# Optimization experiments

Hardware: AMD Instinct MI355X
Metric: run time of the kernel (lower is better)

## Reference

```python
import jax, jax.numpy as jnp
import numpy as np

HID = 512; NH = 8; HD = 64          # attention dims
SH = 8; SD = 32; SDIM = 256          # delta-state dims
NL = 6; FFN = 1536; VOC = 63
THETA = 500000.0; EPS = 1e-6


def rmsnorm(x, w, eps=EPS):
    xf = x.astype(jnp.float32)
    n = xf * jax.lax.rsqrt(jnp.mean(xf * xf, axis=-1, keepdims=True) + eps)
    return (n * w).astype(x.dtype)


def rotate_half(x):
    x1, x2 = jnp.split(x, 2, axis=-1)
    return jnp.concatenate([-x2, x1], axis=-1)


def delta_state(h, S0, Wk, Wv, Wq, Wbw, Wbb, Waw, Wab, Wout, nw, gw):
    # Gated delta-rule associative memory. h: (B,L,HID), S0: (B,SH,SD,SD)
    B, L, _ = h.shape
    k = (h @ Wk.T).reshape(B, L, SH, SD)
    v = (h @ Wv.T).reshape(B, L, SH, SD)
    q = (h @ Wq.T).reshape(B, L, SH, SD)
    beta = jax.nn.sigmoid(h @ Wbw.T + Wbb).reshape(B, L, SH, SD)
    alpha = jax.nn.sigmoid(h @ Waw.T + Wab).reshape(B, L, SH, SD)
    k = k / jnp.maximum(jnp.linalg.norm(k, axis=-1, keepdims=True), 1e-12)
    gate = h @ gw.T  # (B,L,SDIM)
    xs = tuple(jnp.moveaxis(a, 1, 0) for a in (k, v, q, beta, alpha))  # (L,B,SH,SD)

    def step(S, inp):
        k_t, v_t, q_t, b_t, a_t = inp
        S = S * a_t[..., None]                                  # decay rows
        pred = jnp.einsum('bhij,bhj->bhi', S, k_t)
        S = S + jnp.einsum('bhi,bhj->bhij', b_t * (v_t - pred), k_t)
        return S, jnp.einsum('bhij,bhj->bhi', S, q_t)

    S, reads = jax.lax.scan(step, S0, xs)
    ctx = jnp.moveaxis(reads, 0, 1).reshape(B, L, SDIM)
    ctx = rmsnorm(ctx, nw) * jax.nn.silu(gate)
    return ctx @ Wout.T, S


def attention(h, cos, sin, wq, wk, wv, wo):
    B, L, _ = h.shape
    q = (h @ wq.T).reshape(B, L, NH, HD).transpose(0, 2, 1, 3)
    k = (h @ wk.T).reshape(B, L, NH, HD).transpose(0, 2, 1, 3)
    v = (h @ wv.T).reshape(B, L, NH, HD).transpose(0, 2, 1, 3)
    c, s = cos[None, None], sin[None, None]
    q = q * c + rotate_half(q) * s
    k = k * c + rotate_half(k) * s
    scores = jnp.einsum('bhqd,bhkd->bhqk', q, k) / np.float32(np.sqrt(HD))
    mask = jnp.tril(jnp.ones((L, L), bool))
    scores = jnp.where(mask, scores, jnp.float32(-1e9))
    a = jax.nn.softmax(scores, axis=-1)
    o = jnp.einsum('bhqk,bhkd->bhqd', a, v).transpose(0, 2, 1, 3).reshape(B, L, HID)
    return o @ wo.T


def rope_tables(L, dtype):
    inv_freq = 1.0 / THETA ** (np.arange(0, HD, 2, dtype=np.float32) / HD)
    t = np.arange(L, dtype=np.float32)
    freqs = np.outer(t, inv_freq)
    emb = np.concatenate([freqs, freqs], axis=-1)
    return jnp.asarray(np.cos(emb), dtype), jnp.asarray(np.sin(emb), dtype)


def setup_inputs() -> dict:
    key = jax.random.key(0)
    ks = jax.random.split(key, 40)
    p = lambda i, shp: jax.random.normal(ks[i], shp, jnp.float32) * 0.02
    inp = {
        'input_ids': jax.random.randint(ks[0], (4, 1024), 0, VOC),
        'state': jnp.zeros((4, SH, SD, SD), jnp.float32),
        'embed': p(1, (VOC, HID)),
    }
    for j, pre in enumerate(['sr_', 'sw_']):
        b = 2 + j * 10
        inp[pre + 'Wk'] = p(b, (SDIM, HID)); inp[pre + 'Wv'] = p(b + 1, (SDIM, HID))
        inp[pre + 'Wq'] = p(b + 2, (SDIM, HID)); inp[pre + 'Wbw'] = p(b + 3, (SDIM, HID))
        inp[pre + 'Wbb'] = jnp.zeros((SDIM,), jnp.float32)
        inp[pre + 'Waw'] = p(b + 4, (SDIM, HID))
        inp[pre + 'Wab'] = jnp.full((SDIM,), 2.0, jnp.float32)
        inp[pre + 'Wout'] = p(b + 5, (HID, SDIM)); inp[pre + 'nw'] = jnp.ones((SDIM,), jnp.float32)
        inp[pre + 'gw'] = p(b + 6, (SDIM, HID))
    inp['ln1_w'] = jnp.ones((NL, HID), jnp.float32)
    inp['wq'] = p(25, (NL, HID, HID)); inp['wk'] = p(26, (NL, HID, HID))
    inp['wv'] = p(27, (NL, HID, HID)); inp['wo'] = p(28, (NL, HID, HID))
    inp['ln2_w'] = jnp.ones((NL, HID), jnp.float32)
    inp['w_gate'] = p(29, (NL, FFN, HID)); inp['w_up'] = p(30, (NL, FFN, HID))
    inp['w_down'] = p(31, (NL, HID, FFN))
    inp['final_norm_w'] = jnp.ones((HID,), jnp.float32)
    return inp


def reference(input_ids, state, embed,
              sr_Wk, sr_Wv, sr_Wq, sr_Wbw, sr_Wbb, sr_Waw, sr_Wab, sr_Wout, sr_nw, sr_gw,
              sw_Wk, sw_Wv, sw_Wq, sw_Wbw, sw_Wbb, sw_Waw, sw_Wab, sw_Wout, sw_nw, sw_gw,
              ln1_w, wq, wk, wv, wo, ln2_w, w_gate, w_up, w_down, final_norm_w):
    B, L = input_ids.shape
    h = embed[input_ids]
    cos, sin = rope_tables(L, h.dtype)
    read_out, S = delta_state(h, state, sr_Wk, sr_Wv, sr_Wq, sr_Wbw, sr_Wbb, sr_Waw, sr_Wab, sr_Wout, sr_nw, sr_gw)
    h = h + read_out
    for i in range(NL):
        a = attention(rmsnorm(h, ln1_w[i]), cos, sin, wq[i], wk[i], wv[i], wo[i])
        h = h + a
        x = rmsnorm(h, ln2_w[i])
        h = h + (jax.nn.silu(x @ w_gate[i].T) * (x @ w_up[i].T)) @ w_down[i].T
    write_out, S = delta_state(h, S, sw_Wk, sw_Wv, sw_Wq, sw_Wbw, sw_Wbb, sw_Waw, sw_Wab, sw_Wout, sw_nw, sw_gw)
    h = h + write_out
    h = rmsnorm(h, final_norm_w)
    logits = h @ embed.T  # tied embeddings
    return logits, S
```

## Files before the change

### kernel.cpp

```cpp
#include <hip/hip_runtime.h>
#include <hip/hip_bf16.h>
#include <math.h>


#define LSEQ 1024
#define BATCH 4
#define HIDDEN 512
#define NHEAD 8
#define HDIM 64
#define SHEAD 8
#define SDHD 32
#define SDIMM 256
#define FFND 1536
#define VOCN 63
#define ATTS 72

typedef __bf16 bf16;
typedef __attribute__((ext_vector_type(8))) __bf16 bf16x8;
typedef __attribute__((ext_vector_type(4))) float floatx4;

union BF4 { bf16 h[4]; short4 p; };

__device__ __forceinline__ void gload16(const void* g, const void* l) {
    __builtin_amdgcn_global_load_lds(
        (__attribute__((address_space(1))) unsigned int*)(uintptr_t)g,
        (__attribute__((address_space(3))) unsigned int*)(unsigned int)(uintptr_t)l,
        16, 0, 0);
}

__device__ __forceinline__ float sum8(float x) {
    x += __int_as_float(__builtin_amdgcn_mov_dpp(__float_as_int(x), 0xB1, 0xF, 0xF, true));
    x += __int_as_float(__builtin_amdgcn_mov_dpp(__float_as_int(x), 0x4E, 0xF, 0xF, true));
    x += __int_as_float(__builtin_amdgcn_mov_dpp(__float_as_int(x), 0x141, 0xF, 0xF, true));
    return x;
}

__global__ void rope_tables_k(float* __restrict__ cosT, float* __restrict__ sinT) {
    int idx = blockIdx.x * 256 + threadIdx.x;
    int l = idx >> 5, d = idx & 31;
    double ang = (double)l * pow(500000.0, -(double)(2 * d) / 64.0);
    cosT[idx] = (float)cos(ang);
    sinT[idx] = (float)sin(ang);
}

__global__ void embed_k(const int* __restrict__ ids, const float* __restrict__ emb,
                        float* __restrict__ h) {
    int tok = blockIdx.x;
    int id = ids[tok];
    ((float4*)(h + (size_t)tok * HIDDEN))[threadIdx.x] =
        ((const float4*)(emb + (size_t)id * HIDDEN))[threadIdx.x];
}

__global__ void cast_plain(const float* __restrict__ s, bf16* __restrict__ d, int n4) {
    int i = blockIdx.x * 256 + threadIdx.x;
    if (i >= n4) return;
    float4 v = ((const float4*)s)[i];
    BF4 u;
    u.h[0] = (bf16)v.x; u.h[1] = (bf16)v.y; u.h[2] = (bf16)v.z; u.h[3] = (bf16)v.w;
    ((short4*)d)[i] = u.p;
}

__global__ void cast6(const float* s0, const float* s1, const float* s2,
                      const float* s3, const float* s4, const float* s5,
                      bf16* __restrict__ d) {
    int i = blockIdx.x * 256 + threadIdx.x;
    if (i >= 196608) return;
    int which = i >> 15, loc = i & 32767;
    const float* s = which == 0 ? s0 : which == 1 ? s1 : which == 2 ? s2
                    : which == 3 ? s3 : which == 4 ? s4 : s5;
    float4 v = ((const float4*)s)[loc];
    BF4 u;
    u.h[0] = (bf16)v.x; u.h[1] = (bf16)v.y; u.h[2] = (bf16)v.z; u.h[3] = (bf16)v.w;
    ((short4*)d)[i] = u.p;
}

__global__ void cast_qkv(const float* __restrict__ q, const float* __restrict__ k,
                         const float* __restrict__ v, bf16* __restrict__ d) {
    int idx = blockIdx.x * 256 + threadIdx.x;
    if (idx >= 1179648) return;
    int which = idx / 393216;
    int rem = idx - which * 393216;
    const float* s = which == 0 ? q : which == 1 ? k : v;
    int layer = rem >> 16, rr = rem & 65535;
    int r = rr >> 7, c4 = rr & 127;
    float4 x = ((const float4*)s)[rem];
    BF4 u;
    u.h[0] = (bf16)x.x; u.h[1] = (bf16)x.y; u.h[2] = (bf16)x.z; u.h[3] = (bf16)x.w;
    ((short4*)d)[((size_t)layer * 1536 + which * 512 + r) * 128 + c4] = u.p;
}

__global__ void cast_gu(const float* __restrict__ g, const float* __restrict__ uu,
                        bf16* __restrict__ d) {
    int idx = blockIdx.x * 256 + threadIdx.x;
    if (idx >= 2359296) return;
    int which = idx / 1179648;
    int rem = idx - which * 1179648;
    const float* s = which == 0 ? g : uu;
    int layer = rem / 196608, rr = rem - layer * 196608;
    int r = rr >> 7, c4 = rr & 127;
    float4 x = ((const float4*)s)[rem];
    BF4 u;
    u.h[0] = (bf16)x.x; u.h[1] = (bf16)x.y; u.h[2] = (bf16)x.z; u.h[3] = (bf16)x.w;
    ((short4*)d)[((size_t)layer * 3072 + r * 2 + which) * 128 + c4] = u.p;
}

__global__ void cast_embed_pad(const float* __restrict__ s, bf16* __restrict__ d) {
    int i = blockIdx.x * 256 + threadIdx.x;
    int row = i >> 7, c4 = i & 127;
    BF4 u;
    if (row < VOCN) {
        float4 v = ((const float4*)s)[row * 128 + c4];
        u.h[0] = (bf16)v.x; u.h[1] = (bf16)v.y; u.h[2] = (bf16)v.z; u.h[3] = (bf16)v.w;
    } else {
        u.h[0] = (bf16)0.f; u.h[1] = (bf16)0.f; u.h[2] = (bf16)0.f; u.h[3] = (bf16)0.f;
    }
    ((short4*)d)[i] = u.p;
}

__global__ void rmsnorm512(const float* __restrict__ in, const float* __restrict__ w,
                           bf16* __restrict__ out) {
    int row = blockIdx.x, t = threadIdx.x;
    float4 x = ((const float4*)(in + (size_t)row * 512))[t];
    float s = x.x * x.x + x.y * x.y + x.z * x.z + x.w * x.w;
    for (int m = 1; m < 64; m <<= 1) s += __shfl_xor(s, m);
    __shared__ float red[2];
    if ((t & 63) == 0) red[t >> 6] = s;
    __syncthreads();
    float tot = red[0] + red[1];
    float r = rsqrtf(tot * (1.f / 512.f) + 1e-6f);
    float4 wv = ((const float4*)w)[t];
    BF4 u;
    u.h[0] = (bf16)(x.x * r * wv.x); u.h[1] = (bf16)(x.y * r * wv.y);
    u.h[2] = (bf16)(x.z * r * wv.z); u.h[3] = (bf16)(x.w * r * wv.w);
    ((short4*)(out + (size_t)row * 512))[t] = u.p;
}

template <int MODE>
__global__ __launch_bounds__(256) void gemm_bf16(const bf16* __restrict__ A,
                                                 const bf16* __restrict__ B,
                                                 float* __restrict__ C,
                                                 bf16* __restrict__ Cb,
                                                 const float* __restrict__ cosT,
                                                 const float* __restrict__ sinT,
                                                 bf16* __restrict__ Qb,
                                                 bf16* __restrict__ Kb,
                                                 bf16* __restrict__ Vtb,
                                                 int M, int N, int K, int Nreal) {
    __shared__ bf16 As[128 * 64];
    __shared__ bf16 Bs[128 * 64];
    const int tid = threadIdx.x;
    const int wave = tid >> 6, lane = tid & 63;
    const int row0 = blockIdx.y * 128, col0 = blockIdx.x * 128;
    floatx4 acc[4][4];
#pragma unroll
    for (int i = 0; i < 4; ++i)
#pragma unroll
        for (int j = 0; j < 4; ++j) acc[i][j] = (floatx4){0.f, 0.f, 0.f, 0.f};
    const int m0 = (wave & 1) * 64, n0 = (wave >> 1) * 64;
    const int sr = tid >> 3;
    const int ske = ((tid & 7) ^ (sr & 7)) * 8;
    char* AsB = (char*)As;
    char* BsB = (char*)Bs;
    const int ldst = wave * 1024;
    const int ua0 = (((lane >> 4) + 0) ^ (lane & 7)) * 16;
    const int ua1 = (((lane >> 4) + 4) ^ (lane & 7)) * 16;

    for (int k0 = 0; k0 < K; k0 += 64) {
#pragma unroll
        for (int j = 0; j < 4; ++j) {
            gload16(A + (size_t)(row0 + j * 32 + sr) * K + ske + k0,
                    AsB + j * 4096 + ldst);
            gload16(B + (size_t)(col0 + j * 32 + sr) * K + ske + k0,
                    BsB + j * 4096 + ldst);
        }
        __syncthreads();
#pragma unroll
        for (int kk = 0; kk < 2; ++kk) {
            const int uu = kk ? ua1 : ua0;
            bf16x8 af[4], bfr[4];
#pragma unroll
            for (int mi = 0; mi < 4; ++mi)
                af[mi] = *(const bf16x8*)(AsB + (m0 + mi * 16 + (lane & 15)) * 128 + uu);
#pragma unroll
            for (int ni = 0; ni < 4; ++ni)
                bfr[ni] = *(const bf16x8*)(BsB + (n0 + ni * 16 + (lane & 15)) * 128 + uu);
#pragma unroll
            for (int mi = 0; mi < 4; ++mi)
#pragma unroll
                for (int ni = 0; ni < 4; ++ni)
                    acc[mi][ni] = __builtin_amdgcn_mfma_f32_16x16x32_bf16(af[mi], bfr[ni], acc[mi][ni], 0, 0, 0);
        }
        __syncthreads();
    }
    const int cr = (lane >> 4) * 4;
    const int cc = lane & 15;
    if (MODE == 5) {
        int segbase = col0 + n0;
        int seg = segbase >> 9;
        int head = (segbase >> 6) & 7;
#pragma unroll
        for (int mi = 0; mi < 4; ++mi) {
#pragma unroll
            for (int r = 0; r < 4; ++r) {
                int row = row0 + m0 + mi * 16 + cr + r;
                int b = row >> 10, l = row & 1023;
                size_t bh = (size_t)(b * 8 + head);
                float x0 = acc[mi][0][r], x1 = acc[mi][1][r];
                float x2 = acc[mi][2][r], x3 = acc[mi][3][r];
                if (seg < 2) {
                    float c0 = cosT[l * 32 + cc], c1 = cosT[l * 32 + 16 + cc];
                    float s0 = sinT[l * 32 + cc], s1 = sinT[l * 32 + 16 + cc];
                    bf16* dst = (seg == 0 ? Qb : Kb) + bh * 65536 + l * 64;
                    dst[cc]      = (bf16)(x0 * c0 - x2 * s0);
                    dst[16 + cc] = (bf16)(x1 * c1 - x3 * s1);
                    dst[32 + cc] = (bf16)(x2 * c0 + x0 * s0);
                    dst[48 + cc] = (bf16)(x3 * c1 + x1 * s1);
                } else {
                    bf16* dst = Vtb + bh * 65536 + l;
                    dst[(size_t)(cc) * 1024]      = (bf16)x0;
                    dst[(size_t)(16 + cc) * 1024] = (bf16)x1;
                    dst[(size_t)(32 + cc) * 1024] = (bf16)x2;
                    dst[(size_t)(48 + cc) * 1024] = (bf16)x3;
                }
            }
        }
        return;
    }
#pragma unroll
    for (int mi = 0; mi < 4; ++mi) {
#pragma unroll
        for (int ni = 0; ni < 4; ++ni) {
#pragma unroll
            for (int r = 0; r < 4; ++r) {
                int row = row0 + m0 + mi * 16 + cr + r;
                int col = col0 + n0 + ni * 16 + cc;
                float v = acc[mi][ni][r];
                if (MODE == 4) {
                    float o = __shfl_xor(v, 1);
                    if (!(lane & 1)) {
                        float sg = v / (1.f + __expf(-v));
                        Cb[(size_t)row * Nreal + (col >> 1)] = (bf16)(sg * o);
                    }
                } else if (col < Nreal) {
                    size_t off = (size_t)row * Nreal + col;
                    if (MODE == 0) C[off] = v;
                }
            }
        }
    }
}

template <int MODE>
__global__ __launch_bounds__(256) void gemm64_bf16(const bf16* __restrict__ A,
                                                   const bf16* __restrict__ B,
                                                   float* __restrict__ C,
                                                   int M, int N, int K, int Nreal) {
    __shared__ bf16 As[64 * 64];
    __shared__ bf16 Bs[128 * 64];
    const int tid = threadIdx.x;
    const int wave = tid >> 6, lane = tid & 63;
    const int row0 = blockIdx.y * 64, col0 = blockIdx.x * 128;
    floatx4 acc[2][4];
#pragma unroll
    for (int i = 0; i < 2; ++i)
#pragma unroll
        for (int j = 0; j < 4; ++j) acc[i][j] = (floatx4){0.f, 0.f, 0.f, 0.f};
    const int m0 = (wave & 1) * 32, n0 = (wave >> 1) * 64;
    const int sr = tid >> 3;
    const int ske = ((tid & 7) ^ (sr & 7)) * 8;
    char* AsB = (char*)As;
    char* BsB = (char*)Bs;
    const int ldst = wave * 1024;
    const int ua0 = (((lane >> 4) + 0) ^ (lane & 7)) * 16;
    const int ua1 = (((lane >> 4) + 4) ^ (lane & 7)) * 16;

    for (int k0 = 0; k0 < K; k0 += 64) {
#pragma unroll
        for (int j = 0; j < 2; ++j)
            gload16(A + (size_t)(row0 + j * 32 + sr) * K + ske + k0,
                    AsB + j * 4096 + ldst);
#pragma unroll
        for (int j = 0; j < 4; ++j)
            gload16(B + (size_t)(col0 + j * 32 + sr) * K + ske + k0,
                    BsB + j * 4096 + ldst);
        __syncthreads();
#pragma unroll
        for (int kk = 0; kk < 2; ++kk) {
            const int uu = kk ? ua1 : ua0;
            bf16x8 af[2], bfr[4];
#pragma unroll
            for (int mi = 0; mi < 2; ++mi)
                af[mi] = *(const bf16x8*)(AsB + (m0 + mi * 16 + (lane & 15)) * 128 + uu);
#pragma unroll
            for (int ni = 0; ni < 4; ++ni)
                bfr[ni] = *(const bf16x8*)(BsB + (n0 + ni * 16 + (lane & 15)) * 128 + uu);
#pragma unroll
            for (int mi = 0; mi < 2; ++mi)
#pragma unroll
                for (int ni = 0; ni < 4; ++ni)
                    acc[mi][ni] = __builtin_amdgcn_mfma_f32_16x16x32_bf16(af[mi], bfr[ni], acc[mi][ni], 0, 0, 0);
        }
        __syncthreads();
    }
    const int cr = (lane >> 4) * 4;
    const int cc = lane & 15;
#pragma unroll
    for (int mi = 0; mi < 2; ++mi) {
#pragma unroll
        for (int ni = 0; ni < 4; ++ni) {
#pragma unroll
            for (int r = 0; r < 4; ++r) {
                int row = row0 + m0 + mi * 16 + cr + r;
                int col = col0 + n0 + ni * 16 + cc;
                if (col < Nreal) {
                    size_t off = (size_t)row * Nreal + col;
                    float v = acc[mi][ni][r];
                    if (MODE == 0) C[off] = v;
                    else C[off] += v;
                }
            }
        }
    }
}

__global__ __launch_bounds__(256) void attn_mfma(const bf16* __restrict__ Qb,
                                                 const bf16* __restrict__ Kb,
                                                 const bf16* __restrict__ Vtb,
                                                 bf16* __restrict__ O) {
    int qt = blockIdx.x, hh = blockIdx.y, b = blockIdx.z;
    int bh = b * 8 + hh;
    int q0 = qt * 64;
    const bf16* Qg = Qb + ((size_t)bh * 1024 + q0) * 64;
    const bf16* Kg = Kb + (size_t)bh * 1024 * 64;
    const bf16* Vg = Vtb + (size_t)bh * 64 * 1024;
    __shared__ bf16 Qs[64 * ATTS];
    __shared__ bf16 Ks[64 * ATTS];
    __shared__ bf16 Vs[64 * ATTS];
    __shared__ bf16 Ps[64 * ATTS];
    int tid = threadIdx.x, wave = tid >> 6, lane = tid & 63;
    int lr = lane & 15, quad = lane >> 4;

#pragma unroll
    for (int it = 0; it < 2; ++it) {
        int cidx = tid + it * 256;
        int row = cidx >> 3, ch = cidx & 7;
        *(bf16x8*)(Qs + row * ATTS + ch * 8) = *(const bf16x8*)(Qg + row * 64 + ch * 8);
    }
    float mrow[4], lrow[4];
    floatx4 Oacc[4];
#pragma unroll
    for (int r = 0; r < 4; ++r) { mrow[r] = -1e30f; lrow[r] = 0.f; }
#pragma unroll
    for (int d0 = 0; d0 < 4; ++d0) Oacc[d0] = (floatx4){0.f, 0.f, 0.f, 0.f};

    int ntiles = qt + 1;
    for (int t = 0; t < ntiles; ++t) {
        int kv0 = t * 64;
        __syncthreads();
#pragma unroll
        for (int it = 0; it < 2; ++it) {
            int cidx = tid + it * 256;
            int row = cidx >> 3, ch = cidx & 7;
            *(bf16x8*)(Ks + row * ATTS + ch * 8) =
                *(const bf16x8*)(Kg + (size_t)(kv0 + row) * 64 + ch * 8);
            *(bf16x8*)(Vs + row * ATTS + ch * 8) =
                *(const bf16x8*)(Vg + (size_t)row * 1024 + kv0 + ch * 8);
        }
        __syncthreads();
        bf16x8 aq[2];
#pragma unroll
        for (int kc = 0; kc < 2; ++kc)
            aq[kc] = *(const bf16x8*)(Qs + (wave * 16 + lr) * ATTS + kc * 32 + quad * 8);
        floatx4 sacc[4];
#pragma unroll
        for (int n0 = 0; n0 < 4; ++n0) {
            bf16x8 bk0 = *(const bf16x8*)(Ks + (n0 * 16 + lr) * ATTS + quad * 8);
            bf16x8 bk1 = *(const bf16x8*)(Ks + (n0 * 16 + lr) * ATTS + 32 + quad * 8);
            floatx4 z = (floatx4){0.f, 0.f, 0.f, 0.f};
            z = __builtin_amdgcn_mfma_f32_16x16x32_bf16(aq[0], bk0, z, 0, 0, 0);
            sacc[n0] = __builtin_amdgcn_mfma_f32_16x16x32_bf16(aq[1], bk1, z, 0, 0, 0);
        }
        float sv[4][4];
#pragma unroll
        for (int n0 = 0; n0 < 4; ++n0)
#pragma unroll
            for (int r = 0; r < 4; ++r) sv[n0][r] = sacc[n0][r] * 0.125f;
        if (t == ntiles - 1) {
#pragma unroll
            for (int n0 = 0; n0 < 4; ++n0)
#pragma unroll
                for (int r = 0; r < 4; ++r)
                    if (n0 * 16 + lr > wave * 16 + quad * 4 + r) sv[n0][r] = -1e30f;
        }
        float al[4];
#pragma unroll
        for (int r = 0; r < 4; ++r) {
            float tm = fmaxf(fmaxf(sv[0][r], sv[1][r]), fmaxf(sv[2][r], sv[3][r]));
            tm = fmaxf(tm, __shfl_xor(tm, 1));
            tm = fmaxf(tm, __shfl_xor(tm, 2));
            tm = fmaxf(tm, __shfl_xor(tm, 4));
            tm = fmaxf(tm, __shfl_xor(tm, 8));
            float mn = fmaxf(mrow[r], tm);
            al[r] = __expf(mrow[r] - mn);
            mrow[r] = mn;
        }
        float rs[4];
#pragma unroll
        for (int r = 0; r < 4; ++r) rs[r] = 0.f;
#pragma unroll
        for (int n0 = 0; n0 < 4; ++n0)
#pragma unroll
            for (int r = 0; r < 4; ++r) {
                float p = __expf(sv[n0][r] - mrow[r]);
                sv[n0][r] = p;
                rs[r] += p;
            }
#pragma unroll
        for (int r = 0; r < 4; ++r) {
            float t2 = rs[r];
            t2 += __shfl_xor(t2, 1);
            t2 += __shfl_xor(t2, 2);
            t2 += __shfl_xor(t2, 4);
            t2 += __shfl_xor(t2, 8);
            lrow[r] = lrow[r] * al[r] + t2;
        }
#pragma unroll
        for (int d0 = 0; d0 < 4; ++d0)
#pragma unroll
            for (int r = 0; r < 4; ++r) Oacc[d0][r] *= al[r];
#pragma unroll
        for (int n0 = 0; n0 < 4; ++n0)
#pragma unroll
            for (int r = 0; r < 4; ++r)
                Ps[(wave * 16 + quad * 4 + r) * ATTS + n0 * 16 + lr] = (bf16)sv[n0][r];
        bf16x8 ap[2];
#pragma unroll
        for (int kc = 0; kc < 2; ++kc)
            ap[kc] = *(const bf16x8*)(Ps + (wave * 16 + lr) * ATTS + kc * 32 + quad * 8);
#pragma unroll
        for (int d0 = 0; d0 < 4; ++d0) {
            bf16x8 bv0 = *(const bf16x8*)(Vs + (d0 * 16 + lr) * ATTS + quad * 8);
            bf16x8 bv1 = *(const bf16x8*)(Vs + (d0 * 16 + lr) * ATTS + 32 + quad * 8);
            Oacc[d0] = __builtin_amdgcn_mfma_f32_16x16x32_bf16(ap[0], bv0, Oacc[d0], 0, 0, 0);
            Oacc[d0] = __builtin_amdgcn_mfma_f32_16x16x32_bf16(ap[1], bv1, Oacc[d0], 0, 0, 0);
        }
    }
    float inv[4];
#pragma unroll
    for (int r = 0; r < 4; ++r) inv[r] = 1.f / lrow[r];
#pragma unroll
    for (int d0 = 0; d0 < 4; ++d0)
#pragma unroll
        for (int r = 0; r < 4; ++r) {
            int row = b * 1024 + q0 + wave * 16 + quad * 4 + r;
            int col = hh * 64 + d0 * 16 + lr;
            O[(size_t)row * 512 + col] = (bf16)(Oacc[d0][r] * inv[r]);
        }
}

__global__ __launch_bounds__(512, 2) void delta_scan(
    const float* __restrict__ P, const float* __restrict__ S_in,
    const float* __restrict__ bbias, const float* __restrict__ abias,
    float* __restrict__ S_out, float* __restrict__ ctx) {
    int bh = blockIdx.x;
    int b = bh >> 3, hh = bh & 7;
    int tid = threadIdx.x;
    int role = tid >> 8;
    int htid = tid & 255;
    int lane = htid & 63;
    int wv = htid >> 6;
    int ri = wv * 8 + (lane >> 3);
    int c = lane & 7;
    bool cz = (c == 0);
    __shared__ __align__(16) float ks[2][66][36], qs[2][66][36], vs[2][66][36],
                                   bs[2][66][36], as_[2][66][36];
    __shared__ __align__(16) float cpair[2][33][4];
    __shared__ __align__(16) float cs[64][32];
    float4 S = *(const float4*)(S_in + ((size_t)bh * 32 + ri) * 32 + c * 4);

    int sc4 = htid & 7, sr0 = htid >> 3;
    float4 bB = *(const float4*)(bbias + hh * 32 + sc4 * 4);
    float4 bA = *(const float4*)(abias + hh * 32 + sc4 * 4);

    struct Pair {
        float4 k1, k2, q1, q2;
        float a1, a2, b1, b2, bv1, bv2;
        float c12, cq11, cq12, cq22;
    };

    auto dot4 = [](float4 s, float4 k) {
        return fmaf(s.w, k.w, fmaf(s.z, k.z, fmaf(s.y, k.y, s.x * k.x)));
    };

    auto stage_chunk = [&](int c0, int buf) {
        float (*ksH)[36] = ks[buf];
        float (*qsH)[36] = qs[buf];
        float (*vsH)[36] = vs[buf];
        float (*bsH)[36] = bs[buf];
        float (*asH)[36] = as_[buf];
        float (*cpH)[4]  = cpair[buf];
        const float* Pb = P + ((size_t)(b * 1024 + c0) * 1536) + hh * 32 + sc4 * 4;
#pragma unroll
        for (int it = 0; it < 2; ++it) {
            int tok = sr0 + it * 32;
            const float* pg = Pb + (size_t)tok * 1536;
            float4 kv = *(const float4*)(pg);
            float4 vv = *(const float4*)(pg + 256);
            float4 qv = *(const float4*)(pg + 512);
            float4 bv = *(const float4*)(pg + 768);
            float4 av = *(const float4*)(pg + 1024);
            float ss = kv.x * kv.x + kv.y * kv.y + kv.z * kv.z + kv.w * kv.w;
            ss = sum8(ss);
            float rn = 1.f / fmaxf(sqrtf(ss), 1e-12f);
            kv.x *= rn; kv.y *= rn; kv.z *= rn; kv.w *= rn;
            float4 bo, ao;
            bo.x = 1.f / (1.f + __expf(-(bv.x + bB.x)));
            bo.y = 1.f / (1.f + __expf(-(bv.y + bB.y)));
            bo.z = 1.f / (1.f + __expf(-(bv.z + bB.z)));
            bo.w = 1.f / (1.f + __expf(-(bv.w + bB.w)));
            ao.x = 1.f / (1.f + __expf(-(av.x + bA.x)));
            ao.y = 1.f / (1.f + __expf(-(av.y + bA.y)));
            ao.z = 1.f / (1.f + __expf(-(av.z + bA.z)));
            ao.w = 1.f / (1.f + __expf(-(av.w + bA.w)));
            float4 vo;
            vo.x = bo.x * vv.x; vo.y = bo.y * vv.y;
            vo.z = bo.z * vv.z; vo.w = bo.w * vv.w;
            float kq = sum8(kv.x * qv.x + kv.y * qv.y + kv.z * qv.z + kv.w * qv.w);
            float4 ko, qo;
            ko.x = __shfl_xor(kv.x, 8); ko.y = __shfl_xor(kv.y, 8);
            ko.z = __shfl_xor(kv.z, 8); ko.w = __shfl_xor(kv.w, 8);
            qo.x = __shfl_xor(qv.x, 8); qo.y = __shfl_xor(qv.y, 8);
            qo.z = __shfl_xor(qv.z, 8); qo.w = __shfl_xor(qv.w, 8);
            float ckk = sum8(kv.x * ko.x + kv.y * ko.y + kv.z * ko.z + kv.w * ko.w);
            float ckq = sum8(kv.x * qo.x + kv.y * qo.y + kv.z * qo.z + kv.w * qo.w);
            *(float4*)&ksH[tok][sc4 * 4] = kv;
            *(float4*)&vsH[tok][sc4 * 4] = vo;
            *(float4*)&qsH[tok][sc4 * 4] = qv;
            *(float4*)&bsH[tok][sc4 * 4] = bo;
            *(float4*)&asH[tok][sc4 * 4] = ao;
            if ((htid & 7) == 0) {
                int pairi = tok >> 1;
                if (!(tok & 1)) {
                    cpH[pairi][0] = ckk;
                    cpH[pairi][1] = kq;
                    cpH[pairi][2] = ckq;
                } else {
                    cpH[pairi][3] = kq;
                }
            }
        }
    };

    auto scan_chunk = [&](int c0, int buf) {
        float (*ksH)[36] = ks[buf];
        float (*qsH)[36] = qs[buf];
        float (*vsH)[36] = vs[buf];
        float (*bsH)[36] = bs[buf];
        float (*asH)[36] = as_[buf];
        float (*cpH)[4]  = cpair[buf];
        auto loadp = [&](int t, Pair& Pr) {
            Pr.k1 = *(const float4*)&ksH[2 * t][c * 4];
            Pr.k2 = *(const float4*)&ksH[2 * t + 1][c * 4];
            Pr.q1 = *(const float4*)&qsH[2 * t][c * 4];
            Pr.q2 = *(const float4*)&qsH[2 * t + 1][c * 4];
            Pr.a1 = asH[2 * t][ri];  Pr.a2 = asH[2 * t + 1][ri];
            Pr.b1 = bsH[2 * t][ri];  Pr.b2 = bsH[2 * t + 1][ri];
            Pr.bv1 = vsH[2 * t][ri]; Pr.bv2 = vsH[2 * t + 1][ri];
            float4 cp = *(const float4*)&cpH[t][0];
            Pr.c12 = cp.x; Pr.cq11 = cp.y; Pr.cq12 = cp.z; Pr.cq22 = cp.w;
        };
        auto stepp = [&](const Pair& Pr, int t) {
            float d1  = sum8(dot4(S, Pr.k1));
            float d2  = sum8(dot4(S, Pr.k2));
            float dq1 = sum8(dot4(S, Pr.q1));
            float dq2 = sum8(dot4(S, Pr.q2));
            float u1 = fmaf(-(Pr.b1 * Pr.a1), d1, Pr.bv1);
            float au1 = Pr.a2 * u1;
            float A = Pr.a1 * Pr.a2;
            float pred2 = fmaf(au1, Pr.c12, A * d2);
            float u2 = fmaf(-Pr.b2, pred2, Pr.bv2);
            S.x = fmaf(u2, Pr.k2.x, fmaf(au1, Pr.k1.x, A * S.x));
            S.y = fmaf(u2, Pr.k2.y, fmaf(au1, Pr.k1.y, A * S.y));
            S.z = fmaf(u2, Pr.k2.z, fmaf(au1, Pr.k1.z, A * S.z));
            S.w = fmaf(u2, Pr.k2.w, fmaf(au1, Pr.k1.w, A * S.w));
            if (cz) {
                cs[2 * t][ri]     = fmaf(u1, Pr.cq11, Pr.a1 * dq1);
                cs[2 * t + 1][ri] = fmaf(u2, Pr.cq22, fmaf(au1, Pr.cq12, A * dq2));
            }
        };
        Pair PA, PB;
        loadp(0, PA);
        for (int t = 0; t < 32; t += 2) {
            loadp(t + 1, PB);
            stepp(PA, t);
            loadp(t + 2, PA);
            stepp(PB, t + 1);
        }
        int gbase = b * 1024 + c0;
#pragma unroll
        for (int it = 0; it < 2; ++it) {
            int e = lane + it * 64;
            int t = e >> 1, j4 = wv * 2 + (e & 1);
            float4 val = *(const float4*)&cs[t][j4 * 4];
            *(float4*)(ctx + (size_t)(gbase + t) * 256 + hh * 32 + j4 * 4) = val;
        }
    };

    if (role == 1) stage_chunk(0, 0);
    __syncthreads();
    for (int ch = 0; ch < 16; ++ch) {
        if (role == 1) {
            if (ch + 1 < 16) stage_chunk((ch + 1) * 64, (ch + 1) & 1);
        } else {
            scan_chunk(ch * 64, ch & 1);
        }
        __syncthreads();
    }
    if (role == 0)
        *(float4*)(S_out + ((size_t)bh * 32 + ri) * 32 + c * 4) = S;
}

__global__ void ctx_post(const float* __restrict__ ctx, const float* __restrict__ P,
                         const float* __restrict__ nw, bf16* __restrict__ out) {
    int row = blockIdx.x, t = threadIdx.x;
    float4 x = ((const float4*)(ctx + (size_t)row * SDIMM))[t];
    float s = x.x * x.x + x.y * x.y + x.z * x.z + x.w * x.w;
    for (int m = 1; m < 64; m <<= 1) s += __shfl_xor(s, m);
    float r = rsqrtf(s * (1.f / 256.f) + 1e-6f);
    float4 n = ((const float4*)nw)[t];
    float4 g = ((const float4*)(P + (size_t)row * 1536 + 1280))[t];
    BF4 u;
    u.h[0] = (bf16)(x.x * r * n.x * (g.x / (1.f + __expf(-g.x))));
    u.h[1] = (bf16)(x.y * r * n.y * (g.y / (1.f + __expf(-g.y))));
    u.h[2] = (bf16)(x.z * r * n.z * (g.z / (1.f + __expf(-g.z))));
    u.h[3] = (bf16)(x.w * r * n.w * (g.w / (1.f + __expf(-g.w))));
    ((short4*)(out + (size_t)row * SDIMM))[t] = u.p;
}

extern "C" void kernel_launch(void* const* d_in, const int* in_sizes, int n_in,
                              void* d_out, int out_size, void* d_ws, size_t ws_size,
                              hipStream_t stream) {
    (void)in_sizes; (void)n_in; (void)out_size; (void)ws_size;
    const int* ids = (const int*)d_in[0];
    const float* state = (const float*)d_in[1];
    const float* embedw = (const float*)d_in[2];
    auto F = [&](int i) { return (const float*)d_in[i]; };

    char* wsb = (char*)d_ws;
    const size_t MB = 1048576;
    float* H    = (float*)(wsb);
    bf16*  XNbf = (bf16*)(wsb + 8 * MB);
    float* ctxf = (float*)(wsb + 8 * MB);
    bf16*  Hbf  = (bf16*)(wsb + 12 * MB);
    bf16*  ctxb = (bf16*)(wsb + 12 * MB);
    float* P    = (float*)(wsb + 16 * MB);
    bf16*  Obf  = (bf16*)(wsb + 40 * MB);
    bf16*  Qbuf = (bf16*)(wsb + 44 * MB);
    bf16*  Kbuf = (bf16*)(wsb + 48 * MB);
    bf16*  Vtb  = (bf16*)(wsb + 52 * MB);
    bf16*  A1b  = (bf16*)(wsb + 44 * MB);
    float* cosT = (float*)(wsb + 58 * MB);
    float* sinT = cosT + 32768;
    float* Sbuf = sinT + 32768;
    char*  wbase = wsb + 59 * MB;
    bf16* wqkv  = (bf16*)(wbase);
    bf16* wob   = (bf16*)(wbase + 9437184);
    bf16* wgu   = (bf16*)(wbase + 12582912);
    bf16* wdnb  = (bf16*)(wbase + 31457280);
    bf16* wdR   = (bf16*)(wbase + 40894464);
    bf16* woutR = (bf16*)(wbase + 42467328);
    bf16* wdW   = (bf16*)(wbase + 42729472);
    bf16* woutW = (bf16*)(wbase + 44302336);
    bf16* embp  = (bf16*)(wbase + 44564480);

    float* out = (float*)d_out;
    float* logits = out;
    float* Sout = out + 4096 * VOCN;

    auto G0 = [&](const bf16* A, const bf16* B, float* C, int M, int N, int K, int Nreal) {
        gemm_bf16<0><<<dim3(N / 128, M / 128), 256, 0, stream>>>(
            A, B, C, nullptr, nullptr, nullptr, nullptr, nullptr, nullptr, M, N, K, Nreal);
    };
    auto G4 = [&](const bf16* A, const bf16* B, bf16* Cb, int M, int N, int K, int Nreal) {
        gemm_bf16<4><<<dim3(N / 128, M / 128), 256, 0, stream>>>(
            A, B, nullptr, Cb, nullptr, nullptr, nullptr, nullptr, nullptr, M, N, K, Nreal);
    };
    auto G5 = [&](const bf16* A, const bf16* B, int M, int N, int K) {
        gemm_bf16<5><<<dim3(N / 128, M / 128), 256, 0, stream>>>(
            A, B, nullptr, nullptr, cosT, sinT, Qbuf, Kbuf, Vtb, M, N, K, N);
    };
    auto G1s = [&](const bf16* A, const bf16* B, float* C, int M, int N, int K) {
        gemm64_bf16<1><<<dim3(N / 128, M / 64), 256, 0, stream>>>(A, B, C, M, N, K, N);
    };
    auto G0s = [&](const bf16* A, const bf16* B, float* C, int M, int N, int K, int Nreal) {
        gemm64_bf16<0><<<dim3(N / 128, M / 64), 256, 0, stream>>>(A, B, C, M, N, K, Nreal);
    };
    auto CP = [&](const float* s, bf16* d, int n4) {
        cast_plain<<<(n4 + 255) / 256, 256, 0, stream>>>(s, d, n4);
    };

    cast_qkv<<<4608, 256, 0, stream>>>(F(24), F(25), F(26), wqkv);
    CP(F(27), wob, 393216);
    cast_gu<<<9216, 256, 0, stream>>>(F(29), F(30), wgu);
    CP(F(31), wdnb, 1179648);
    cast6<<<768, 256, 0, stream>>>(F(3), F(4), F(5), F(6), F(8), F(12), wdR);
    CP(F(10), woutR, 32768);
    cast6<<<768, 256, 0, stream>>>(F(13), F(14), F(15), F(16), F(18), F(22), wdW);
    CP(F(20), woutW, 32768);
    cast_embed_pad<<<64, 256, 0, stream>>>(embedw, embp);

    rope_tables_k<<<128, 256, 0, stream>>>(cosT, sinT);
    embed_k<<<4096, 128, 0, stream>>>(ids, embedw, H);

    CP(H, Hbf, 524288);
    G0(Hbf, wdR, P, 4096, 1536, 512, 1536);
    delta_scan<<<32, 512, 0, stream>>>(P, state, F(7), F(9), Sbuf, ctxf);
    ctx_post<<<4096, 64, 0, stream>>>(ctxf, P, F(11), ctxb);
    G1s(ctxb, woutR, H, 4096, 512, 256);

    for (int i = 0; i < 6; ++i) {
        rmsnorm512<<<4096, 128, 0, stream>>>(H, F(23) + (size_t)i * 512, XNbf);
        G5(XNbf, wqkv + (size_t)i * 1536 * 512, 4096, 1536, 512);
        attn_mfma<<<dim3(16, 8, 4), 256, 0, stream>>>(Qbuf, Kbuf, Vtb, Obf);
        G1s(Obf, wob + (size_t)i * 512 * 512, H, 4096, 512, 512);
        rmsnorm512<<<4096, 128, 0, stream>>>(H, F(28) + (size_t)i * 512, XNbf);
        G4(XNbf, wgu + (size_t)i * 3072 * 512, A1b, 4096, 3072, 512, 1536);
        G1s(A1b, wdnb + (size_t)i * 512 * 1536, H, 4096, 512, 1536);
    }

    CP(H, Hbf, 524288);
    G0(Hbf, wdW, P, 4096, 1536, 512, 1536);
    delta_scan<<<32, 512, 0, stream>>>(P, Sbuf, F(17), F(19), Sout, ctxf);
    ctx_post<<<4096, 64, 0, stream>>>(ctxf, P, F(21), ctxb);
    G1s(ctxb, woutW, H, 4096, 512, 256);

    rmsnorm512<<<4096, 128, 0, stream>>>(H, F(32), XNbf);
    G0s(XNbf, embp, logits, 4096, 128, 512, VOCN);
}
```

Before: 1.304 ms.

## Fuse RMSNorm into GEMM A-loading and merge setup casts into one kernel

Folds the 11 weight-cast, rope-table and embedding kernels into a single cast_all launch. It also makes the main GEMM read fp32 activations directly, computing per-row RMS norms in a prologue and applying norm and weight scaling while converting to bf16 in LDS. This removes the separate rmsnorm and H-cast kernels and their bf16 round trips. In exchange, A tiles are now loaded through registers instead of async global-to-LDS copies. Every column block also rereads and renormalizes full fp32 rows, so A traffic grows and load/compute overlap may drop.

After: 1.674 ms. 1.28x slower.

```diff
diff --git a/kernel.cpp b/kernel.cpp
--- a/kernel.cpp
+++ b/kernel.cpp
@@ -35,86 +35,89 @@
     return x;
 }
 
-__global__ void rope_tables_k(float* __restrict__ cosT, float* __restrict__ sinT) {
-    int idx = blockIdx.x * 256 + threadIdx.x;
-    int l = idx >> 5, d = idx & 31;
-    double ang = (double)l * pow(500000.0, -(double)(2 * d) / 64.0);
-    cosT[idx] = (float)cos(ang);
-    sinT[idx] = (float)sin(ang);
-}
-
-__global__ void embed_k(const int* __restrict__ ids, const float* __restrict__ emb,
-                        float* __restrict__ h) {
-    int tok = blockIdx.x;
-    int id = ids[tok];
-    ((float4*)(h + (size_t)tok * HIDDEN))[threadIdx.x] =
-        ((const float4*)(emb + (size_t)id * HIDDEN))[threadIdx.x];
-}
-
-__global__ void cast_plain(const float* __restrict__ s, bf16* __restrict__ d, int n4) {
-    int i = blockIdx.x * 256 + threadIdx.x;
-    if (i >= n4) return;
+struct CastArgs {
+    const float *wq, *wk, *wv, *wob, *wg, *wu, *wdn;
+    const float *r0, *r1, *r2, *r3, *r4, *r5, *woutR;
+    const float *w0, *w1, *w2, *w3, *w4, *w5, *woutW;
+    const float *emb; const int *ids;
+    bf16 *wqkvD, *wobD, *wguD, *wdnbD, *wdRD, *woutRD, *wdWD, *woutWD, *embpD;
+    float *cosT, *sinT, *H;
+};
+
+__device__ __forceinline__ void cast4(const float* s, bf16* d, int i) {
     float4 v = ((const float4*)s)[i];
     BF4 u;
     u.h[0] = (bf16)v.x; u.h[1] = (bf16)v.y; u.h[2] = (bf16)v.z; u.h[3] = (bf16)v.w;
     ((short4*)d)[i] = u.p;
 }
 
-__global__ void cast6(const float* s0, const float* s1, const float* s2,
-                      const float* s3, const float* s4, const float* s5,
-                      bf16* __restrict__ d) {
-    int i = blockIdx.x * 256 + threadIdx.x;
-    if (i >= 196608) return;
-    int which = i >> 15, loc = i & 32767;
-    const float* s = which == 0 ? s0 : which == 1 ? s1 : which == 2 ? s2
-                    : which == 3 ? s3 : which == 4 ? s4 : s5;
-    float4 v = ((const float4*)s)[loc];
-    BF4 u;
-    u.h[0] = (bf16)v.x; u.h[1] = (bf16)v.y; u.h[2] = (bf16)v.z; u.h[3] = (bf16)v.w;
-    ((short4*)d)[i] = u.p;
-}
-
-__global__ void cast_qkv(const float* __restrict__ q, const float* __restrict__ k,
-                         const float* __restrict__ v, bf16* __restrict__ d) {
-    int idx = blockIdx.x * 256 + threadIdx.x;
-    if (idx >= 1179648) return;
-    int which = idx / 393216;
-    int rem = idx - which * 393216;
-    const float* s = which == 0 ? q : which == 1 ? k : v;
-    int layer = rem >> 16, rr = rem & 65535;
-    int r = rr >> 7, c4 = rr & 127;
-    float4 x = ((const float4*)s)[rem];
-    BF4 u;
-    u.h[0] = (bf16)x.x; u.h[1] = (bf16)x.y; u.h[2] = (bf16)x.z; u.h[3] = (bf16)x.w;
-    ((short4*)d)[((size_t)layer * 1536 + which * 512 + r) * 128 + c4] = u.p;
-}
-
-__global__ void cast_gu(const float* __restrict__ g, const float* __restrict__ uu,
-                        bf16* __restrict__ d) {
-    int idx = blockIdx.x * 256 + threadIdx.x;
-    if (idx >= 2359296) return;
-    int which = idx / 1179648;
-    int rem = idx - which * 1179648;
-    const float* s = which == 0 ? g : uu;
-    int layer = rem / 196608, rr = rem - layer * 196608;
-    int r = rr >> 7, c4 = rr & 127;
-    float4 x = ((const float4*)s)[rem];
-    BF4 u;
-    u.h[0] = (bf16)x.x; u.h[1] = (bf16)x.y; u.h[2] = (bf16)x.z; u.h[3] = (bf16)x.w;
-    ((short4*)d)[((size_t)layer * 3072 + r * 2 + which) * 128 + c4] = u.p;
-}
-
-__global__ void cast_embed_pad(const float* __restrict__ s, bf16* __restrict__ d) {
-    int i = blockIdx.x * 256 + threadIdx.x;
-    int row = i >> 7, c4 = i & 127;
-    BF4 u;
-    if (row < VOCN) {
-        float4 v = ((const float4*)s)[row * 128 + c4];
-        u.h[0] = (bf16)v.x; u.h[1] = (bf16)v.y; u.h[2] = (bf16)v.z; u.h[3] = (bf16)v.w;
+__global__ void cast_all(CastArgs a) {
+    int bx = blockIdx.x, tid = threadIdx.x;
+    if (bx < 4608) {
+        int idx = bx * 256 + tid;
+        int which = idx / 393216;
+        int rem = idx - which * 393216;
+        const float* s = which == 0 ? a.wq : which == 1 ? a.wk : a.wv;
+        int layer = rem >> 16, rr = rem & 65535;
+        int r = rr >> 7, c4 = rr & 127;
+        float4 x = ((const float4*)s)[rem];
+        BF4 u;
+        u.h[0] = (bf16)x.x; u.h[1] = (bf16)x.y; u.h[2] = (bf16)x.z; u.h[3] = (bf16)x.w;
+        ((short4*)a.wqkvD)[((size_t)layer * 1536 + which * 512 + r) * 128 + c4] = u.p;
+    } else if (bx < 6144) {
+        cast4(a.wob, a.wobD, (bx - 4608) * 256 + tid);
+    } else if (bx < 15360) {
+        int idx = (bx - 6144) * 256 + tid;
+        int which = idx / 1179648;
+        int rem = idx - which * 1179648;
+        const float* s = which == 0 ? a.wg : a.wu;
+        int layer = rem / 196608, rr = rem - layer * 196608;
+        int r = rr >> 7, c4 = rr & 127;
+        float4 x = ((const float4*)s)[rem];
+        BF4 u;
+        u.h[0] = (bf16)x.x; u.h[1] = (bf16)x.y; u.h[2] = (bf16)x.z; u.h[3] = (bf16)x.w;
+        ((short4*)a.wguD)[((size_t)layer * 3072 + r * 2 + which) * 128 + c4] = u.p;
+    } else if (bx < 19968) {
+        cast4(a.wdn, a.wdnbD, (bx - 15360) * 256 + tid);
+    } else if (bx < 20736) {
+        int i = (bx - 19968) * 256 + tid;
+        int which = i >> 15, loc = i & 32767;
+        const float* s = which == 0 ? a.r0 : which == 1 ? a.r1 : which == 2 ? a.r2
+                        : which == 3 ? a.r3 : which == 4 ? a.r4 : a.r5;
+        cast4(s - (size_t)0, a.wdRD + (size_t)which * 131072, loc);
+    } else if (bx < 20864) {
+        cast4(a.woutR, a.woutRD, (bx - 20736) * 256 + tid);
+    } else if (bx < 21632) {
+        int i = (bx - 20864) * 256 + tid;
+        int which = i >> 15, loc = i & 32767;
+        const float* s = which == 0 ? a.w0 : which == 1 ? a.w1 : which == 2 ? a.w2
+                        : which == 3 ? a.w3 : which == 4 ? a.w4 : a.w5;
+        cast4(s, a.wdWD + (size_t)which * 131072, loc);
+    } else if (bx < 21760) {
+        cast4(a.woutW, a.woutWD, (bx - 21632) * 256 + tid);
+    } else if (bx < 21824) {
+        int i = (bx - 21760) * 256 + tid;
+        int row = i >> 7, c4 = i & 127;
+        BF4 u;
+        if (row < VOCN) {
+            float4 v = ((const float4*)a.emb)[row * 128 + c4];
+            u.h[0] = (bf16)v.x; u.h[1] = (bf16)v.y; u.h[2] = (bf16)v.z; u.h[3] = (bf16)v.w;
+        } else {
+            u.h[0] = (bf16)0.f; u.h[1] = (bf16)0.f; u.h[2] = (bf16)0.f; u.h[3] = (bf16)0.f;
+        }
+        ((short4*)a.embpD)[i] = u.p;
+    } else if (bx < 21952) {
+        int idx = (bx - 21824) * 256 + tid;
+        int l = idx >> 5, d = idx & 31;
+        double ang = (double)l * pow(500000.0, -(double)(2 * d) / 64.0);
+        a.cosT[idx] = (float)cos(ang);
+        a.sinT[idx] = (float)sin(ang);
     } else {
-        u.h[0] = (bf16)0.f; u.h[1] = (bf16)0.f; u.h[2] = (bf16)0.f; u.h[3] = (bf16)0.f;
-    }
-    ((short4*)d)[i] = u.p;
+        int tok = (bx - 21952) * 2 + (tid >> 7);
+        int id = a.ids[tok];
+        ((float4*)(a.H + (size_t)tok * HIDDEN))[tid & 127] =
+            ((const float4*)(a.emb + (size_t)id * HIDDEN))[tid & 127];
+    }
 }
 
 __global__ void rmsnorm512(const float* __restrict__ in, const float* __restrict__ w,
@@ -135,9 +138,10 @@
     ((short4*)(out + (size_t)row * 512))[t] = u.p;
 }
 
-template <int MODE>
-__global__ __launch_bounds__(256) void gemm_bf16(const bf16* __restrict__ A,
+template <int MODE, int NORM>
+__global__ __launch_bounds__(256) void gemm_bf16(const float* __restrict__ A,
                                                  const bf16* __restrict__ B,
+                                                 const float* __restrict__ W,
                                                  float* __restrict__ C,
                                                  bf16* __restrict__ Cb,
                                                  const float* __restrict__ cosT,
@@ -146,8 +150,10 @@
                                                  bf16* __restrict__ Kb,
                                                  bf16* __restrict__ Vtb,
                                                  int M, int N, int K, int Nreal) {
-    __shared__ bf16 As[128 * 64];
+    __shared__ bf16 As[128 * 72];
     __shared__ bf16 Bs[128 * 64];
+    __shared__ float rnorm[128];
+    __shared__ float wn[512];
     const int tid = threadIdx.x;
     const int wave = tid >> 6, lane = tid & 63;
     const int row0 = blockIdx.y * 128, col0 = blockIdx.x * 128;
@@ -159,31 +165,63 @@
     const int m0 = (wave & 1) * 64, n0 = (wave >> 1) * 64;
     const int sr = tid >> 3;
     const int ske = ((tid & 7) ^ (sr & 7)) * 8;
-    char* AsB = (char*)As;
     char* BsB = (char*)Bs;
-    const int ldst = wave * 1024;
-    const int ua0 = (((lane >> 4) + 0) ^ (lane & 7)) * 16;
-    const int ua1 = (((lane >> 4) + 4) ^ (lane & 7)) * 16;
+    const int ldstB = wave * 1024;
+    const int uaB0 = (((lane >> 4) + 0) ^ (lane & 7)) * 16;
+    const int uaB1 = (((lane >> 4) + 4) ^ (lane & 7)) * 16;
+    const int ar = tid >> 1, ah = tid & 1;
+
+    float rn = 1.f;
+    if (NORM) {
+        for (int i = tid; i < 128; i += 256)
+            ((float4*)wn)[i] = ((const float4*)W)[i];
+        const float* arow = A + (size_t)(row0 + ar) * K + ah * 256;
+        float s = 0.f;
+#pragma unroll 8
+        for (int j = 0; j < 64; ++j) {
+            float4 v = ((const float4*)arow)[j];
+            s += v.x * v.x + v.y * v.y + v.z * v.z + v.w * v.w;
+        }
+        s += __shfl_xor(s, 1);
+        if (!ah) rnorm[ar] = rsqrtf(s * (1.f / 512.f) + 1e-6f);
+        __syncthreads();
+        rn = rnorm[ar];
+    }
 
     for (int k0 = 0; k0 < K; k0 += 64) {
-#pragma unroll
-        for (int j = 0; j < 4; ++j) {
-            gload16(A + (size_t)(row0 + j * 32 + sr) * K + ske + k0,
-                    AsB + j * 4096 + ldst);
+        const float* ap = A + (size_t)(row0 + ar) * K + k0 + ah * 32;
+#pragma unroll
+        for (int jj = 0; jj < 4; ++jj) {
+            float4 v0 = ((const float4*)ap)[jj * 2];
+            float4 v1 = ((const float4*)ap)[jj * 2 + 1];
+            if (NORM) {
+                const float* wp = &wn[k0 + ah * 32 + jj * 8];
+                float4 w0 = *(const float4*)wp;
+                float4 w1 = *(const float4*)(wp + 4);
+                v0.x *= rn * w0.x; v0.y *= rn * w0.y; v0.z *= rn * w0.z; v0.w *= rn * w0.w;
+                v1.x *= rn * w1.x; v1.y *= rn * w1.y; v1.z *= rn * w1.z; v1.w *= rn * w1.w;
+            }
+            bf16x8 pk;
+            pk[0] = (bf16)v0.x; pk[1] = (bf16)v0.y; pk[2] = (bf16)v0.z; pk[3] = (bf16)v0.w;
+            pk[4] = (bf16)v1.x; pk[5] = (bf16)v1.y; pk[6] = (bf16)v1.z; pk[7] = (bf16)v1.w;
+            *(bf16x8*)(As + ar * 72 + ah * 32 + jj * 8) = pk;
+        }
+#pragma unroll
+        for (int j = 0; j < 4; ++j)
             gload16(B + (size_t)(col0 + j * 32 + sr) * K + ske + k0,
-                    BsB + j * 4096 + ldst);
-        }
+                    BsB + j * 4096 + ldstB);
         __syncthreads();
 #pragma unroll
         for (int kk = 0; kk < 2; ++kk) {
-            const int uu = kk ? ua1 : ua0;
+            const int uuB = kk ? uaB1 : uaB0;
             bf16x8 af[4], bfr[4];
 #pragma unroll
             for (int mi = 0; mi < 4; ++mi)
-                af[mi] = *(const bf16x8*)(AsB + (m0 + mi * 16 + (lane & 15)) * 128 + uu);
+                af[mi] = *(const bf16x8*)(As + (m0 + mi * 16 + (lane & 15)) * 72 +
+                                          (kk * 4 + (lane >> 4)) * 8);
 #pragma unroll
             for (int ni = 0; ni < 4; ++ni)
-                bfr[ni] = *(const bf16x8*)(BsB + (n0 + ni * 16 + (lane & 15)) * 128 + uu);
+                bfr[ni] = *(const bf16x8*)(BsB + (n0 + ni * 16 + (lane & 15)) * 128 + uuB);
 #pragma unroll
             for (int mi = 0; mi < 4; ++mi)
 #pragma unroll
@@ -651,7 +689,6 @@
     float* H    = (float*)(wsb);
     bf16*  XNbf = (bf16*)(wsb + 8 * MB);
     float* ctxf = (float*)(wsb + 8 * MB);
-    bf16*  Hbf  = (bf16*)(wsb + 12 * MB);
     bf16*  ctxb = (bf16*)(wsb + 12 * MB);
     float* P    = (float*)(wsb + 16 * MB);
     bf16*  Obf  = (bf16*)(wsb + 40 * MB);
@@ -677,17 +714,20 @@
     float* logits = out;
     float* Sout = out + 4096 * VOCN;
 
-    auto G0 = [&](const bf16* A, const bf16* B, float* C, int M, int N, int K, int Nreal) {
-        gemm_bf16<0><<<dim3(N / 128, M / 128), 256, 0, stream>>>(
-            A, B, C, nullptr, nullptr, nullptr, nullptr, nullptr, nullptr, M, N, K, Nreal);
-    };
-    auto G4 = [&](const bf16* A, const bf16* B, bf16* Cb, int M, int N, int K, int Nreal) {
-        gemm_bf16<4><<<dim3(N / 128, M / 128), 256, 0, stream>>>(
-            A, B, nullptr, Cb, nullptr, nullptr, nullptr, nullptr, nullptr, M, N, K, Nreal);
-    };
-    auto G5 = [&](const bf16* A, const bf16* B, int M, int N, int K) {
-        gemm_bf16<5><<<dim3(N / 128, M / 128), 256, 0, stream>>>(
-            A, B, nullptr, nullptr, cosT, sinT, Qbuf, Kbuf, Vtb, M, N, K, N);
+    auto G0f = [&](const float* A, const bf16* B, float* C, int M, int N, int K, int Nreal) {
+        gemm_bf16<0, 0><<<dim3(N / 128, M / 128), 256, 0, stream>>>(
+            A, B, nullptr, C, nullptr, nullptr, nullptr, nullptr, nullptr, nullptr,
+            M, N, K, Nreal);
+    };
+    auto G4n = [&](const float* A, const float* W, const bf16* B, bf16* Cb,
+                   int M, int N, int K, int Nreal) {
+        gemm_bf16<4, 1><<<dim3(N / 128, M / 128), 256, 0, stream>>>(
+            A, B, W, nullptr, Cb, nullptr, nullptr, nullptr, nullptr, nullptr,
+            M, N, K, Nreal);
+    };
+    auto G5n = [&](const float* A, const float* W, const bf16* B, int M, int N, int K) {
+        gemm_bf16<5, 1><<<dim3(N / 128, M / 128), 256, 0, stream>>>(
+            A, B, W, nullptr, nullptr, cosT, sinT, Qbuf, Kbuf, Vtb, M, N, K, N);
     };
     auto G1s = [&](const bf16* A, const bf16* B, float* C, int M, int N, int K) {
         gemm64_bf16<1><<<dim3(N / 128, M / 64), 256, 0, stream>>>(A, B, C, M, N, K, N);
@@ -695,41 +735,35 @@
     auto G0s = [&](const bf16* A, const bf16* B, float* C, int M, int N, int K, int Nreal) {
         gemm64_bf16<0><<<dim3(N / 128, M / 64), 256, 0, stream>>>(A, B, C, M, N, K, Nreal);
     };
-    auto CP = [&](const float* s, bf16* d, int n4) {
-        cast_plain<<<(n4 + 255) / 256, 256, 0, stream>>>(s, d, n4);
-    };
-
-    cast_qkv<<<4608, 256, 0, stream>>>(F(24), F(25), F(26), wqkv);
-    CP(F(27), wob, 393216);
-    cast_gu<<<9216, 256, 0, stream>>>(F(29), F(30), wgu);
-    CP(F(31), wdnb, 1179648);
-    cast6<<<768, 256, 0, stream>>>(F(3), F(4), F(5), F(6), F(8), F(12), wdR);
-    CP(F(10), woutR, 32768);
-    cast6<<<768, 256, 0, stream>>>(F(13), F(14), F(15), F(16), F(18), F(22), wdW);
-    CP(F(20), woutW, 32768);
-    cast_embed_pad<<<64, 256, 0, stream>>>(embedw, embp);
-
-    rope_tables_k<<<128, 256, 0, stream>>>(cosT, sinT);
-    embed_k<<<4096, 128, 0, stream>>>(ids, embedw, H);
-
-    CP(H, Hbf, 524288);
-    G0(Hbf, wdR, P, 4096, 1536, 512, 1536);
+
+    CastArgs ca;
+    ca.wq = F(24); ca.wk = F(25); ca.wv = F(26); ca.wob = F(27);
+    ca.wg = F(29); ca.wu = F(30); ca.wdn = F(31);
+    ca.r0 = F(3); ca.r1 = F(4); ca.r2 = F(5); ca.r3 = F(6); ca.r4 = F(8); ca.r5 = F(12);
+    ca.woutR = F(10);
+    ca.w0 = F(13); ca.w1 = F(14); ca.w2 = F(15); ca.w3 = F(16); ca.w4 = F(18); ca.w5 = F(22);
+    ca.woutW = F(20);
+    ca.emb = embedw; ca.ids = ids;
+    ca.wqkvD = wqkv; ca.wobD = wob; ca.wguD = wgu; ca.wdnbD = wdnb;
+    ca.wdRD = wdR; ca.woutRD = woutR; ca.wdWD = wdW; ca.woutWD = woutW;
+    ca.embpD = embp; ca.cosT = cosT; ca.sinT = sinT; ca.H = H;
+    cast_all<<<24000, 256, 0, stream>>>(ca);
+
+    G0f(H, wdR, P, 4096, 1536, 512, 1536);
     delta_scan<<<32, 512, 0, stream>>>(P, state, F(7), F(9), Sbuf, ctxf);
     ctx_post<<<4096, 64, 0, stream>>>(ctxf, P, F(11), ctxb);
     G1s(ctxb, woutR, H, 4096, 512, 256);
 
     for (int i = 0; i < 6; ++i) {
-        rmsnorm512<<<4096, 128, 0, stream>>>(H, F(23) + (size_t)i * 512, XNbf);
-        G5(XNbf, wqkv + (size_t)i * 1536 * 512, 4096, 1536, 512);
+        G5n(H, F(23) + (size_t)i * 512, wqkv + (size_t)i * 1536 * 512, 4096, 1536, 512);
         attn_mfma<<<dim3(16, 8, 4), 256, 0, stream>>>(Qbuf, Kbuf, Vtb, Obf);
         G1s(Obf, wob + (size_t)i * 512 * 512, H, 4096, 512, 512);
-        rmsnorm512<<<4096, 128, 0, stream>>>(H, F(28) + (size_t)i * 512, XNbf);
-        G4(XNbf, wgu + (size_t)i * 3072 * 512, A1b, 4096, 3072, 512, 1536);
+        G4n(H, F(28) + (size_t)i * 512, wgu + (size_t)i * 3072 * 512, A1b,
+            4096, 3072, 512, 1536);
         G1s(A1b, wdnb + (size_t)i * 512 * 1536, H, 4096, 512, 1536);
     }
 
-    CP(H, Hbf, 524288);
-    G0(Hbf, wdW, P, 4096, 1536, 512, 1536);
+    G0f(H, wdW, P, 4096, 1536, 512, 1536);
     delta_scan<<<32, 512, 0, stream>>>(P, Sbuf, F(17), F(19), Sout, ctxf);
     ctx_post<<<4096, 64, 0, stream>>>(ctxf, P, F(21), ctxb);
     G1s(ctxb, woutW, H, 4096, 512, 256);
```
